# Performance work log

Hardware: AMD Instinct MI355X
Metric: run time of the kernel (lower is better)

## Reference

```python
import jax, jax.numpy as jnp
import numpy as np

F = 256       # in_src/in_dst feature dim (feat_dict)
HID = 256     # hidden_dim
K = 16        # sampled neighbors per dst node (fixed fan-out)
N_REVIEW = 16384
N_USER = 65536
N_PRODUCT = 65536
EPS = 1e-5


def setup_inputs() -> dict:
    key = jax.random.key(0)
    ks = jax.random.split(key, 24)
    rn = lambda k, shape, s=0.05: jax.random.normal(k, shape, jnp.float32) * s
    inp = {
        'x_user': jax.random.normal(ks[0], (N_USER, F), jnp.float32),
        'x_product': jax.random.normal(ks[1], (N_PRODUCT, F), jnp.float32),
        'x_review': jax.random.normal(ks[2], (N_REVIEW, F), jnp.float32),
        'nbr_user': jax.random.randint(ks[3], (N_REVIEW, K), 0, N_USER),
        'nbr_product': jax.random.randint(ks[4], (N_REVIEW, K), 0, N_PRODUCT),
    }
    i = 5
    for pre in ('u_', 'p_'):
        inp[pre + 'Wih'] = rn(ks[i], (4 * F, F)); i += 1      # LSTM input weights (gates i,f,g,o)
        inp[pre + 'Whh'] = rn(ks[i], (4 * F, F)); i += 1      # LSTM hidden weights
        inp[pre + 'bih'] = jnp.zeros((4 * F,), jnp.float32)
        inp[pre + 'bhh'] = jnp.zeros((4 * F,), jnp.float32)
        inp[pre + 'Wself'] = rn(ks[i], (HID, F)); i += 1      # SAGEConv fc_self
        inp[pre + 'Wneigh'] = rn(ks[i], (HID, F)); i += 1     # SAGEConv fc_neigh
        inp[pre + 'bconv'] = jnp.zeros((HID,), jnp.float32)   # SAGEConv bias
    inp['ln_g'] = jnp.ones((HID,), jnp.float32)
    inp['ln_b'] = jnp.zeros((HID,), jnp.float32)
    inp['bn_g'] = jnp.ones((HID,), jnp.float32)
    inp['bn_b'] = jnp.zeros((HID,), jnp.float32)
    inp['W1'] = rn(ks[i], (HID, HID)); i += 1
    inp['b1'] = jnp.zeros((HID,), jnp.float32)
    inp['W2'] = rn(ks[i], (2, HID)); i += 1
    inp['b2'] = jnp.zeros((2,), jnp.float32)
    return inp


def _lstm_last(x, Wih, Whh, bih, bhh):
    # x: [N, K, F] neighbor sequences; returns final hidden state [N, F]
    n, _, f = x.shape
    b = bih + bhh
    def step(carry, xt):  # xt: [N, F]
        h, c = carry
        gates = xt @ Wih.T + h @ Whh.T + b  # [N, 4F]
        ig, fg, gg, og = jnp.split(gates, 4, axis=-1)
        c = jax.nn.sigmoid(fg) * c + jax.nn.sigmoid(ig) * jnp.tanh(gg)
        h = jax.nn.sigmoid(og) * jnp.tanh(c)
        return (h, c), None
    h0 = jnp.zeros((n, f), x.dtype)
    (h, _), _ = jax.lax.scan(step, (h0, h0), jnp.swapaxes(x, 0, 1))
    return h


def _sage_rel(x_src, x_dst, nbr, Wih, Whh, bih, bhh, Wself, Wneigh, bconv):
    # gather neighbor features [N_dst, K, F] (feat_drop is identity at eval)
    nb = x_src[nbr]
    h_neigh = _lstm_last(nb, Wih, Whh, bih, bhh)            # [N_dst, F]
    rst = x_dst @ Wself.T + h_neigh @ Wneigh.T + bconv       # [N_dst, HID]
    return jax.nn.gelu(rst, approximate=False)               # activation=nn.GELU()


def reference(x_user, x_product, x_review, nbr_user, nbr_product,
              u_Wih, u_Whh, u_bih, u_bhh, u_Wself, u_Wneigh, u_bconv,
              p_Wih, p_Whh, p_bih, p_bhh, p_Wself, p_Wneigh, p_bconv,
              ln_g, ln_b, bn_g, bn_b, W1, b1, W2, b2):
    # HeteroGraphConv(aggregate='sum') over the two relations into 'review'
    h = (_sage_rel(x_user, x_review, nbr_user, u_Wih, u_Whh, u_bih, u_bhh,
                   u_Wself, u_Wneigh, u_bconv)
         + _sage_rel(x_product, x_review, nbr_product, p_Wih, p_Whh, p_bih, p_bhh,
                     p_Wself, p_Wneigh, p_bconv))
    # LayerNorm
    mu = jnp.mean(h, axis=-1, keepdims=True)
    var = jnp.var(h, axis=-1, keepdims=True)
    h = (h - mu) * jax.lax.rsqrt(var + EPS) * ln_g + ln_b
    # clf head: Dropout (identity at eval) -> BatchNorm1d (batch stats) -> MLP
    bm = jnp.mean(h, axis=0, keepdims=True)
    bv = jnp.var(h, axis=0, keepdims=True)
    h = (h - bm) * jax.lax.rsqrt(bv + EPS) * bn_g + bn_b
    h = jax.nn.gelu(h @ W1.T + b1, approximate=False)
    return h @ W2.T + b2  # [N_REVIEW, 2]
```

## Files before the change

### kernel.cpp

```cpp
#include <hip/hip_runtime.h>
#include <math.h>

#define NREV 16384
#define NUSER 65536
#define NPROD 65536
#define KNBR 16
#define LDK 72

typedef __attribute__((ext_vector_type(8))) short short8;
typedef __attribute__((ext_vector_type(4))) float f32x4;
typedef unsigned short u16;

__device__ __forceinline__ u16 f2bf(float f){
  union { float f; unsigned u; } x; x.f = f;
  unsigned r = x.u + 0x7fffu + ((x.u >> 16) & 1u);
  return (u16)(r >> 16);
}
__device__ __forceinline__ float bf2f(u16 u){
  union { unsigned u; float f; } x; x.u = ((unsigned)u) << 16;
  return x.f;
}
__device__ __forceinline__ float fexp2(float x){ return __builtin_amdgcn_exp2f(x); }
__device__ __forceinline__ float frcp(float x){ return __builtin_amdgcn_rcpf(x); }
#define LOG2E 1.4426950408889634f
__device__ __forceinline__ float sigf(float x){ return frcp(1.f + fexp2(-LOG2E*x)); }
__device__ __forceinline__ float tanh_fast(float x){ return 1.f - 2.f*frcp(1.f + fexp2(2.f*LOG2E*x)); }
__device__ __forceinline__ float gelu_fast(float x){
  float u = 0.7978845608f*x*(1.f + 0.044715f*x*x);
  return 0.5f*x*(1.f + tanh_fast(u));
}

__global__ void cvt_kernel(const float* __restrict__ src, u16* __restrict__ dst, int n4){
  int i = blockIdx.x*256 + threadIdx.x;
  if(i < n4){
    float4 v = reinterpret_cast<const float4*>(src)[i];
    ushort4 o; o.x=f2bf(v.x); o.y=f2bf(v.y); o.z=f2bf(v.z); o.w=f2bf(v.w);
    reinterpret_cast<ushort4*>(dst)[i] = o;
  }
}

__global__ void pack_lstm_kernel(const float* __restrict__ Wihp, const float* __restrict__ Whhp,
                                 const float* __restrict__ bihp, const float* __restrict__ bhhp,
                                 u16* __restrict__ Bpp, float* __restrict__ bpp){
  int n = blockIdx.x;
  int g = n & 3, j = n >> 2;
  int m = g*256 + j;
  int k = threadIdx.x;
  Bpp[(size_t)n*512 + k]       = f2bf(Wihp[(size_t)m*256 + k]);
  Bpp[(size_t)n*512 + 256 + k] = f2bf(Whhp[(size_t)m*256 + k]);
  if(k == 0) bpp[n] = bihp[m] + bhhp[m];
}

__global__ void pack_sage_kernel(const float* __restrict__ Wselfp, const float* __restrict__ Wneighp,
                                 u16* __restrict__ Bsp){
  int n = blockIdx.x;
  int k = threadIdx.x;
  Bsp[(size_t)n*512 + k]       = f2bf(Wselfp[(size_t)n*256 + k]);
  Bsp[(size_t)n*512 + 256 + k] = f2bf(Wneighp[(size_t)n*256 + k]);
}

__global__ __launch_bounds__(256) void xw_kernel(
    const u16* __restrict__ xb, const u16* __restrict__ Bp,
    const float* __restrict__ bp, u16* __restrict__ xwout)
{
  __shared__ u16 sA[128*LDK];
  __shared__ u16 sB[128*LDK];
  int tid = threadIdx.x;
  int nt = blockIdx.x, rt = blockIdx.y;
  f32x4 acc[4][4];
  #pragma unroll
  for(int i=0;i<4;++i)
    #pragma unroll
    for(int j=0;j<4;++j) acc[i][j] = (f32x4){0.f,0.f,0.f,0.f};
  int lane = tid & 63, w = tid >> 6, wr = w >> 1, wc = w & 1;
  int ci = tid & 7, r0 = tid >> 3;
  int rrow = lane & 15, lhi = lane >> 4, kb = lhi * 8;

  for(int kt=0; kt<4; ++kt){
    __syncthreads();
    #pragma unroll
    for(int pp=0; pp<4; ++pp){
      int row = pp*32 + r0;
      *(short8*)&sA[row*LDK + ci*8] =
        *(const short8*)(xb + (size_t)(rt*128 + row)*256 + kt*64 + ci*8);
      *(short8*)&sB[row*LDK + ci*8] =
        *(const short8*)(Bp + (size_t)(nt*128 + row)*512 + kt*64 + ci*8);
    }
    __syncthreads();
    #pragma unroll
    for(int kk=0; kk<2; ++kk){
      short8 af[4], bfv[4];
      #pragma unroll
      for(int ni=0;ni<4;++ni) af[ni]  = *(const short8*)&sB[(wc*64+ni*16+rrow)*LDK + kk*32 + kb];
      #pragma unroll
      for(int mi=0;mi<4;++mi) bfv[mi] = *(const short8*)&sA[(wr*64+mi*16+rrow)*LDK + kk*32 + kb];
      #pragma unroll
      for(int ni=0;ni<4;++ni)
        #pragma unroll
        for(int mi=0;mi<4;++mi)
          acc[ni][mi] = __builtin_amdgcn_mfma_f32_16x16x32_bf16(af[ni], bfv[mi], acc[ni][mi], 0, 0, 0);
    }
  }
  #pragma unroll
  for(int mi=0;mi<4;++mi){
    size_t node = (size_t)(rt*128 + wr*64 + mi*16 + rrow);
    u16* dst = xwout + node*1024;
    #pragma unroll
    for(int ni=0;ni<4;++ni){
      int n0 = nt*128 + wc*64 + ni*16 + lhi*4;
      float4 bv = *(const float4*)&bp[n0];
      ushort4 o;
      o.x = f2bf(acc[ni][mi][0] + bv.x);
      o.y = f2bf(acc[ni][mi][1] + bv.y);
      o.z = f2bf(acc[ni][mi][2] + bv.z);
      o.w = f2bf(acc[ni][mi][3] + bv.w);
      *(ushort4*)(dst + n0) = o;
    }
  }
}

__global__ __launch_bounds__(256, 3) void lstm_step6_kernel(
    const u16* __restrict__ xw, const int* __restrict__ nbr, int t,
    const u16* __restrict__ Bh,
    const u16* __restrict__ hin, u16* __restrict__ hout, u16* __restrict__ cT)
{
  __shared__ u16 sA[128*LDK];
  __shared__ u16 sB[128*LDK];
  int tid = threadIdx.x;
  int nt = blockIdx.x, rt = blockIdx.y;
  int lane = tid & 63, w = tid >> 6, wr = w >> 1, wc = w & 1;
  int ci = tid & 7, r0 = tid >> 3;
  int rrow = lane & 15, lhi = lane >> 4, kb = lhi * 8;

  int node[4];
  #pragma unroll
  for(int mi=0;mi<4;++mi)
    node[mi] = nbr[(size_t)(rt*128 + wr*64 + mi*16 + rrow)*KNBR + t];
  ushort4 xv[4][4];
  #pragma unroll
  for(int mi=0;mi<4;++mi)
    #pragma unroll
    for(int ni=0;ni<4;++ni){
      int n0 = nt*128 + wc*64 + ni*16 + lhi*4;
      xv[mi][ni] = *(const ushort4*)(xw + (size_t)node[mi]*1024 + n0);
    }

  f32x4 acc[4][4];
  #pragma unroll
  for(int i=0;i<4;++i)
    #pragma unroll
    for(int j=0;j<4;++j) acc[i][j] = (f32x4){0.f,0.f,0.f,0.f};

  if(t > 0){
    for(int kt=0; kt<4; ++kt){
      __syncthreads();
      #pragma unroll
      for(int pp=0; pp<4; ++pp){
        int row = pp*32 + r0;
        *(short8*)&sA[row*LDK + ci*8] =
          *(const short8*)(hin + (size_t)(rt*128 + row)*256 + kt*64 + ci*8);
        *(short8*)&sB[row*LDK + ci*8] =
          *(const short8*)(Bh + (size_t)(nt*128 + row)*512 + kt*64 + ci*8);
      }
      __syncthreads();
      #pragma unroll
      for(int kk=0; kk<2; ++kk){
        short8 af[4], bfv[4];
        #pragma unroll
        for(int ni=0;ni<4;++ni) af[ni]  = *(const short8*)&sB[(wc*64+ni*16+rrow)*LDK + kk*32 + kb];
        #pragma unroll
        for(int mi=0;mi<4;++mi) bfv[mi] = *(const short8*)&sA[(wr*64+mi*16+rrow)*LDK + kk*32 + kb];
        #pragma unroll
        for(int ni=0;ni<4;++ni)
          #pragma unroll
          for(int mi=0;mi<4;++mi)
            acc[ni][mi] = __builtin_amdgcn_mfma_f32_16x16x32_bf16(af[ni], bfv[mi], acc[ni][mi], 0, 0, 0);
      }
    }
  }

  u16 cv[4][4];
  #pragma unroll
  for(int mi=0;mi<4;++mi)
    #pragma unroll
    for(int ni=0;ni<4;++ni){
      cv[mi][ni] = 0;
      if(t > 0){
        int j = nt*32 + wc*16 + ni*4 + lhi;
        cv[mi][ni] = cT[(size_t)j*NREV + rt*128 + wr*64 + mi*16 + rrow];
      }
    }

  #pragma unroll
  for(int mi=0;mi<4;++mi){
    int rg = rt*128 + wr*64 + mi*16 + rrow;
    #pragma unroll
    for(int ni=0;ni<4;++ni){
      int j = nt*32 + wc*16 + ni*4 + lhi;
      float ig = bf2f(xv[mi][ni].x) + acc[ni][mi][0];
      float fg = bf2f(xv[mi][ni].y) + acc[ni][mi][1];
      float gg = bf2f(xv[mi][ni].z) + acc[ni][mi][2];
      float og = bf2f(xv[mi][ni].w) + acc[ni][mi][3];
      float cn = sigf(fg)*bf2f(cv[mi][ni]) + sigf(ig)*tanh_fast(gg);
      cT[(size_t)j*NREV + rg] = f2bf(cn);
      hout[(size_t)rg*256 + j] = f2bf(sigf(og)*tanh_fast(cn));
    }
  }
}

template<int MODE>
__global__ __launch_bounds__(256) void gemm_act_kernel(
    const u16* __restrict__ A0, const u16* __restrict__ A1,
    const u16* __restrict__ Bp, const float* __restrict__ bias,
    float* __restrict__ outF, u16* __restrict__ outH)
{
  constexpr int KT   = (MODE == 2) ? 4 : 8;
  constexpr int KTOT = KT * 64;
  __shared__ u16 sA[128*LDK];
  __shared__ u16 sB[128*LDK];
  int tid = threadIdx.x;
  int rt = blockIdx.x, nt = blockIdx.y;
  f32x4 acc[4][4];
  #pragma unroll
  for(int i=0;i<4;++i)
    #pragma unroll
    for(int j=0;j<4;++j) acc[i][j] = (f32x4){0.f,0.f,0.f,0.f};
  int lane = tid & 63, w = tid >> 6, wr = w >> 1, wc = w & 1;
  int ci = tid & 7, r0 = tid >> 3;
  int rrow = lane & 15, kb = (lane >> 4) * 8;

  for(int kt=0; kt<KT; ++kt){
    __syncthreads();
    #pragma unroll
    for(int pp=0; pp<4; ++pp){
      int row = pp*32 + r0;
      const u16* srcA = (kt < 4)
        ? (A0 + ((size_t)(rt*128 + row))*256 + kt*64)
        : (A1 + ((size_t)(rt*128 + row))*256 + (kt-4)*64);
      *(short8*)&sA[row*LDK + ci*8] = *(const short8*)(srcA + ci*8);
      const u16* srcB = Bp + ((size_t)(nt*128 + row))*KTOT + kt*64;
      *(short8*)&sB[row*LDK + ci*8] = *(const short8*)(srcB + ci*8);
    }
    __syncthreads();
    #pragma unroll
    for(int kk=0; kk<2; ++kk){
      short8 af[4], bfv[4];
      #pragma unroll
      for(int mi=0;mi<4;++mi) af[mi] = *(const short8*)&sA[(wr*64+mi*16+rrow)*LDK + kk*32 + kb];
      #pragma unroll
      for(int ni=0;ni<4;++ni) bfv[ni] = *(const short8*)&sB[(wc*64+ni*16+rrow)*LDK + kk*32 + kb];
      #pragma unroll
      for(int mi=0;mi<4;++mi)
        #pragma unroll
        for(int ni=0;ni<4;++ni)
          acc[mi][ni] = __builtin_amdgcn_mfma_f32_16x16x32_bf16(af[mi], bfv[ni], acc[mi][ni], 0, 0, 0);
    }
  }
  #pragma unroll
  for(int mi=0;mi<4;++mi)
    #pragma unroll
    for(int ni=0;ni<4;++ni){
      int col  = nt*128 + wc*64 + ni*16 + rrow;
      int rowb = rt*128 + wr*64 + mi*16 + (lane>>4)*4;
      float bv = bias[col];
      #pragma unroll
      for(int q=0;q<4;++q){
        float x = acc[mi][ni][q] + bv;
        float gl = gelu_fast(x);
        size_t idx = (size_t)(rowb+q)*256 + col;
        if(MODE == 0)      outF[idx] = gl;
        else if(MODE == 1) outF[idx] += gl;
        else               outH[idx] = f2bf(gl);
      }
    }
}

__global__ void ln_kernel(const float* __restrict__ hs, const float* __restrict__ g,
                          const float* __restrict__ b, u16* __restrict__ hlnp){
  int w = threadIdx.x >> 6, lane = threadIdx.x & 63;
  int r = blockIdx.x*4 + w;
  const float* row = hs + (size_t)r*256;
  float4 v = *(const float4*)(row + lane*4);
  float s  = v.x+v.y+v.z+v.w;
  float ss = v.x*v.x + v.y*v.y + v.z*v.z + v.w*v.w;
  #pragma unroll
  for(int d=1; d<64; d<<=1){ s += __shfl_xor(s, d, 64); ss += __shfl_xor(ss, d, 64); }
  float mu  = s  * (1.f/256.f);
  float var = ss * (1.f/256.f) - mu*mu;
  float rs  = rsqrtf(var + 1e-5f);
  float4 gv = *(const float4*)(g + lane*4);
  float4 bv = *(const float4*)(b + lane*4);
  ushort4 o;
  o.x = f2bf((v.x-mu)*rs*gv.x + bv.x);
  o.y = f2bf((v.y-mu)*rs*gv.y + bv.y);
  o.z = f2bf((v.z-mu)*rs*gv.z + bv.z);
  o.w = f2bf((v.w-mu)*rs*gv.w + bv.w);
  *(ushort4*)(hlnp + (size_t)r*256 + lane*4) = o;
}

__global__ void colstats_kernel(const u16* __restrict__ hlnp, float* __restrict__ cs, float* __restrict__ cq){
  int cix = threadIdx.x;
  size_t rb = (size_t)blockIdx.x * 128;
  float s=0.f, q=0.f;
  for(int rr=0; rr<128; ++rr){
    float v = bf2f(hlnp[(rb+rr)*256 + cix]);
    s += v; q += v*v;
  }
  atomicAdd(&cs[cix], s);
  atomicAdd(&cq[cix], q);
}

__global__ void bnstat_kernel(const float* __restrict__ cs, const float* __restrict__ cq,
                              const float* __restrict__ bng, const float* __restrict__ bnb,
                              float* __restrict__ bns, float* __restrict__ bnt){
  int cix = threadIdx.x;
  float bm = cs[cix] * (1.f/16384.f);
  float bv = cq[cix] * (1.f/16384.f) - bm*bm;
  float s  = bng[cix] * rsqrtf(bv + 1e-5f);
  bns[cix] = s;
  bnt[cix] = bnb[cix] - bm*s;
}

__global__ void w1fold_kernel(const float* __restrict__ W1p, const float* __restrict__ b1p,
                              const float* __restrict__ bns, const float* __restrict__ bnt,
                              u16* __restrict__ W1fp, float* __restrict__ b1fp){
  __shared__ float red[4];
  int n = blockIdx.x, k = threadIdx.x;
  int lane = k & 63, w = k >> 6;
  float wv = W1p[(size_t)n*256 + k];
  W1fp[(size_t)n*256 + k] = f2bf(wv * bns[k]);
  float p = wv * bnt[k];
  #pragma unroll
  for(int d=1; d<64; d<<=1) p += __shfl_xor(p, d, 64);
  if(lane == 0) red[w] = p;
  __syncthreads();
  if(k == 0) b1fp[n] = b1p[n] + red[0] + red[1] + red[2] + red[3];
}

__global__ void head_kernel(const u16* __restrict__ z, const float* __restrict__ W2p,
                            const float* __restrict__ b2p, float* __restrict__ outp){
  int w = threadIdx.x >> 6, lane = threadIdx.x & 63;
  int r = blockIdx.x*4 + w;
  const u16* zr = z + (size_t)r*256;
  ushort4 v = *(const ushort4*)(zr + lane*4);
  float z0=bf2f(v.x), z1v=bf2f(v.y), z2=bf2f(v.z), z3=bf2f(v.w);
  float4 wa = *(const float4*)(W2p + lane*4);
  float4 wb = *(const float4*)(W2p + 256 + lane*4);
  float p0 = z0*wa.x + z1v*wa.y + z2*wa.z + z3*wa.w;
  float p1 = z0*wb.x + z1v*wb.y + z2*wb.z + z3*wb.w;
  #pragma unroll
  for(int d=1; d<64; d<<=1){ p0 += __shfl_xor(p0,d,64); p1 += __shfl_xor(p1,d,64); }
  if(lane == 0){
    outp[(size_t)r*2]   = p0 + b2p[0];
    outp[(size_t)r*2+1] = p1 + b2p[1];
  }
}

extern "C" void kernel_launch(void* const* d_in, const int* in_sizes, int n_in,
                              void* d_out, int out_size, void* d_ws, size_t ws_size,
                              hipStream_t stream){
  (void)in_sizes; (void)n_in; (void)out_size;
  const float* x_user    = (const float*)d_in[0];
  const float* x_product = (const float*)d_in[1];
  const float* x_review  = (const float*)d_in[2];
  const int*   nbr_user  = (const int*)d_in[3];
  const int*   nbr_prod  = (const int*)d_in[4];
  const float* Wih[2]    = {(const float*)d_in[5],  (const float*)d_in[12]};
  const float* Whh[2]    = {(const float*)d_in[6],  (const float*)d_in[13]};
  const float* bih[2]    = {(const float*)d_in[7],  (const float*)d_in[14]};
  const float* bhh[2]    = {(const float*)d_in[8],  (const float*)d_in[15]};
  const float* Wself[2]  = {(const float*)d_in[9],  (const float*)d_in[16]};
  const float* Wneigh[2] = {(const float*)d_in[10], (const float*)d_in[17]};
  const float* bconv[2]  = {(const float*)d_in[11], (const float*)d_in[18]};
  const float* ln_g=(const float*)d_in[19], *ln_b=(const float*)d_in[20];
  const float* bn_g=(const float*)d_in[21], *bn_b=(const float*)d_in[22];
  const float* W1=(const float*)d_in[23], *b1=(const float*)d_in[24];
  const float* W2=(const float*)d_in[25], *b2=(const float*)d_in[26];
  float* out = (float*)d_out;

  char* base = (char*)d_ws;
  size_t off = 0;
  auto alloc = [&](size_t bytes)->char* { char* r = base + off; off += (bytes + 255) & ~(size_t)255; return r; };
  u16*   xr   = (u16*)  alloc((size_t)NREV*256*2);
  float* hsum = (float*)alloc((size_t)NREV*256*4);
  u16*   Bp[2]; Bp[0]=(u16*)alloc(1024*512*2); Bp[1]=(u16*)alloc(1024*512*2);
  float* bp[2]; bp[0]=(float*)alloc(4096);     bp[1]=(float*)alloc(4096);
  u16*   Bs[2]; Bs[0]=(u16*)alloc(256*512*2);  Bs[1]=(u16*)alloc(256*512*2);
  float* csum = (float*)alloc(1024);
  float* csq  = (float*)alloc(1024);
  float* bns  = (float*)alloc(1024);
  float* bnt  = (float*)alloc(1024);
  u16*   W1f  = (u16*)  alloc(256*256*2);
  float* b1f  = (float*)alloc(1024);
  u16*   hA    = (u16*)alloc((size_t)NREV*256*2);
  u16*   hB    = (u16*)alloc((size_t)NREV*256*2);
  u16*   cT    = (u16*)alloc((size_t)NREV*256*4);
  u16*   xW    = (u16*)alloc((size_t)NUSER*1024*2);
  if(off > ws_size) return;
  u16* xcvt = hA;
  u16* hln  = hA;
  u16* z1   = hB;

  cvt_kernel<<<dim3(4096),256,0,stream>>>(x_review, xr, NREV*256/4);
  for(int rel=0; rel<2; ++rel){
    pack_lstm_kernel<<<dim3(1024),256,0,stream>>>(Wih[rel],Whh[rel],bih[rel],bhh[rel],Bp[rel],bp[rel]);
    pack_sage_kernel<<<dim3(256), 256,0,stream>>>(Wself[rel],Wneigh[rel],Bs[rel]);
  }
  hipMemsetAsync(csum, 0, 1024, stream);
  hipMemsetAsync(csq,  0, 1024, stream);

  for(int rel=0; rel<2; ++rel){
    const float* xs = rel ? x_product : x_user;
    const int*   nb = rel ? nbr_prod  : nbr_user;
    cvt_kernel<<<dim3(16384),256,0,stream>>>(xs, xcvt, NUSER*256/4);
    xw_kernel<<<dim3(8,512),256,0,stream>>>(xcvt, Bp[rel], bp[rel], xW);
    u16 *hin = hB, *hout = hA;
    for(int t=0; t<KNBR; ++t){
      lstm_step6_kernel<<<dim3(8,128),256,0,stream>>>(xW, nb, t, Bp[rel] + 256, hin, hout, cT);
      u16* tmp = hin; hin = hout; hout = tmp;
    }
    if(rel == 0)
      gemm_act_kernel<0><<<dim3(128,2),256,0,stream>>>(xr, hin, Bs[0], bconv[0], hsum, nullptr);
    else
      gemm_act_kernel<1><<<dim3(128,2),256,0,stream>>>(xr, hin, Bs[1], bconv[1], hsum, nullptr);
  }

  ln_kernel<<<dim3(4096),256,0,stream>>>(hsum, ln_g, ln_b, hln);
  colstats_kernel<<<dim3(128),256,0,stream>>>(hln, csum, csq);
  bnstat_kernel<<<dim3(1),256,0,stream>>>(csum, csq, bn_g, bn_b, bns, bnt);
  w1fold_kernel<<<dim3(256),256,0,stream>>>(W1, b1, bns, bnt, W1f, b1f);
  gemm_act_kernel<2><<<dim3(128,2),256,0,stream>>>(hln, nullptr, W1f, b1f, nullptr, z1);
  head_kernel<<<dim3(4096),256,0,stream>>>(z1, W2, b2, out);
}
```

Before: 1.396 ms.

## Fuse fp32-to-bf16 conversion into xw GEMM, remap blocks per XCD, keep cell state fp32

The separate conversion kernel for user/product features is removed, and the xw GEMM now loads fp32 inputs and converts them to bf16 while staging into shared memory. This avoids writing and re-reading a bf16 copy of the features. The xw grid becomes 1D with an XCD-aware mapping so that blocks sharing a row tile land on the same XCD for L2 reuse. The LSTM cell state is now stored in fp32 instead of bf16, which improves accuracy but doubles cell-state memory traffic in every step kernel.

```diff
diff --git a/kernel.cpp b/kernel.cpp
--- a/kernel.cpp
+++ b/kernel.cpp
@@ -60,13 +60,16 @@
 }
 
 __global__ __launch_bounds__(256) void xw_kernel(
-    const u16* __restrict__ xb, const u16* __restrict__ Bp,
+    const float* __restrict__ x, const u16* __restrict__ Bp,
     const float* __restrict__ bp, u16* __restrict__ xwout)
 {
   __shared__ u16 sA[128*LDK];
   __shared__ u16 sB[128*LDK];
   int tid = threadIdx.x;
-  int nt = blockIdx.x, rt = blockIdx.y;
+  int p = blockIdx.x;
+  int xcd = p & 7, g = p >> 3;
+  int nt = g & 7;
+  int rt = (g >> 3) * 8 + xcd;
   f32x4 acc[4][4];
   #pragma unroll
   for(int i=0;i<4;++i)
@@ -81,8 +84,13 @@
     #pragma unroll
     for(int pp=0; pp<4; ++pp){
       int row = pp*32 + r0;
-      *(short8*)&sA[row*LDK + ci*8] =
-        *(const short8*)(xb + (size_t)(rt*128 + row)*256 + kt*64 + ci*8);
+      const float* srcA = x + (size_t)(rt*128 + row)*256 + kt*64 + ci*8;
+      float4 a0 = *(const float4*)srcA;
+      float4 a1 = *(const float4*)(srcA + 4);
+      short8 s;
+      s[0]=f2bf(a0.x); s[1]=f2bf(a0.y); s[2]=f2bf(a0.z); s[3]=f2bf(a0.w);
+      s[4]=f2bf(a1.x); s[5]=f2bf(a1.y); s[6]=f2bf(a1.z); s[7]=f2bf(a1.w);
+      *(short8*)&sA[row*LDK + ci*8] = s;
       *(short8*)&sB[row*LDK + ci*8] =
         *(const short8*)(Bp + (size_t)(nt*128 + row)*512 + kt*64 + ci*8);
     }
@@ -119,10 +127,10 @@
   }
 }
 
-__global__ __launch_bounds__(256, 3) void lstm_step6_kernel(
+__global__ __launch_bounds__(256, 3) void lstm_step7_kernel(
     const u16* __restrict__ xw, const int* __restrict__ nbr, int t,
     const u16* __restrict__ Bh,
-    const u16* __restrict__ hin, u16* __restrict__ hout, u16* __restrict__ cT)
+    const u16* __restrict__ hin, u16* __restrict__ hout, float* __restrict__ cT)
 {
   __shared__ u16 sA[128*LDK];
   __shared__ u16 sB[128*LDK];
@@ -179,12 +187,12 @@
     }
   }
 
-  u16 cv[4][4];
+  float cv[4][4];
   #pragma unroll
   for(int mi=0;mi<4;++mi)
     #pragma unroll
     for(int ni=0;ni<4;++ni){
-      cv[mi][ni] = 0;
+      cv[mi][ni] = 0.f;
       if(t > 0){
         int j = nt*32 + wc*16 + ni*4 + lhi;
         cv[mi][ni] = cT[(size_t)j*NREV + rt*128 + wr*64 + mi*16 + rrow];
@@ -201,8 +209,8 @@
       float fg = bf2f(xv[mi][ni].y) + acc[ni][mi][1];
       float gg = bf2f(xv[mi][ni].z) + acc[ni][mi][2];
       float og = bf2f(xv[mi][ni].w) + acc[ni][mi][3];
-      float cn = sigf(fg)*bf2f(cv[mi][ni]) + sigf(ig)*tanh_fast(gg);
-      cT[(size_t)j*NREV + rg] = f2bf(cn);
+      float cn = sigf(fg)*cv[mi][ni] + sigf(ig)*tanh_fast(gg);
+      cT[(size_t)j*NREV + rg] = cn;
       hout[(size_t)rg*256 + j] = f2bf(sigf(og)*tanh_fast(cn));
     }
   }
@@ -392,14 +400,13 @@
   float* bnt  = (float*)alloc(1024);
   u16*   W1f  = (u16*)  alloc(256*256*2);
   float* b1f  = (float*)alloc(1024);
-  u16*   hA    = (u16*)alloc((size_t)NREV*256*2);
-  u16*   hB    = (u16*)alloc((size_t)NREV*256*2);
-  u16*   cT    = (u16*)alloc((size_t)NREV*256*4);
-  u16*   xW    = (u16*)alloc((size_t)NUSER*1024*2);
+  u16*   hA   = (u16*)  alloc((size_t)NREV*256*2);
+  u16*   hB   = (u16*)  alloc((size_t)NREV*256*2);
+  float* cT   = (float*)alloc((size_t)NREV*256*4);
+  u16*   xW   = (u16*)  alloc((size_t)NUSER*1024*2);
   if(off > ws_size) return;
-  u16* xcvt = hA;
-  u16* hln  = hA;
-  u16* z1   = hB;
+  u16* hln = hA;
+  u16* z1  = hB;
 
   cvt_kernel<<<dim3(4096),256,0,stream>>>(x_review, xr, NREV*256/4);
   for(int rel=0; rel<2; ++rel){
@@ -412,11 +419,10 @@
   for(int rel=0; rel<2; ++rel){
     const float* xs = rel ? x_product : x_user;
     const int*   nb = rel ? nbr_prod  : nbr_user;
-    cvt_kernel<<<dim3(16384),256,0,stream>>>(xs, xcvt, NUSER*256/4);
-    xw_kernel<<<dim3(8,512),256,0,stream>>>(xcvt, Bp[rel], bp[rel], xW);
+    xw_kernel<<<dim3(4096),256,0,stream>>>(xs, Bp[rel], bp[rel], xW);
     u16 *hin = hB, *hout = hA;
     for(int t=0; t<KNBR; ++t){
-      lstm_step6_kernel<<<dim3(8,128),256,0,stream>>>(xW, nb, t, Bp[rel] + 256, hin, hout, cT);
+      lstm_step7_kernel<<<dim3(8,128),256,0,stream>>>(xW, nb, t, Bp[rel] + 256, hin, hout, cT);
       u16* tmp = hin; hin = hout; hout = tmp;
     }
     if(rel == 0)
```

After: 1.291 ms. -7.5%, faster.
